# Performance work log

Measured on AMD Instinct MI355X. Metric: run time of the kernel, lower is better.

## Reference

```python
import jax, jax.numpy as jnp
import numpy as np

NUM_HIST = 4
INTERVAL = 5
PROG_THRESH = 2.0

B = 32          # scenarios
AGENTS_PER = 10 # agents per scenario
A = B * AGENTS_PER
T = 32          # future intervals
P = 20000       # polylines
NG = 2000       # polygons
L = 180         # raw trajectory length (L//INTERVAL = 36 >= T+1)


def setup_inputs() -> dict:
    key = jax.random.key(0)
    ks = jax.random.split(key, 8)
    polyline_batch = jnp.sort(jax.random.randint(ks[0], (P,), 0, B, dtype=jnp.int32))
    polyline_position = jax.random.normal(ks[1], (P, 2), dtype=jnp.float32) * 50.0
    polyline_heading = jax.random.uniform(ks[2], (P,), dtype=jnp.float32) * 2.0 * np.pi
    edge_row1 = jax.random.randint(ks[3], (P,), 0, NG, dtype=jnp.int32)
    polyline_to_polygon_edge_index = jnp.stack([jnp.arange(P, dtype=jnp.int32), edge_row1])
    polygon_on_route_mask = jax.random.randint(ks[4], (NG,), 0, 2) > 0
    agent_ptr = (jnp.arange(B + 1, dtype=jnp.int32) * AGENTS_PER)
    agent_infer_position = jax.random.normal(ks[5], (A, NUM_HIST + T, 2), dtype=jnp.float32) * 50.0
    agent_batch = jnp.repeat(jnp.arange(B, dtype=jnp.int32), AGENTS_PER)
    agent_position = jax.random.normal(ks[6], (A, L, 2), dtype=jnp.float32) * 50.0
    return {
        "polyline_batch": polyline_batch,
        "polyline_position": polyline_position,
        "polyline_heading": polyline_heading,
        "polyline_to_polygon_edge_index": polyline_to_polygon_edge_index,
        "polygon_on_route_mask": polygon_on_route_mask,
        "agent_ptr": agent_ptr,
        "agent_infer_position": agent_infer_position,
        "agent_batch": agent_batch,
        "agent_position": agent_position,
    }


def _local_x(points, centers, cos_h, sin_h):
    # points [E,2]; centers [P,2]; returns x_local, y_local each [E,P]
    dx = points[:, None, 0] - centers[None, :, 0]
    dy = points[:, None, 1] - centers[None, :, 1]
    x = cos_h[None, :] * dx + sin_h[None, :] * dy
    y = -sin_h[None, :] * dx + cos_h[None, :] * dy
    return x, y


def _progress(pos, pos_pre, pos_batch, poly_pos, cos_h, sin_h, on_route, poly_batch, t):
    # dense equivalent of mask-build -> dense_to_sparse -> gather -> scatter_min
    x, y = _local_x(pos, poly_pos, cos_h, sin_h)          # [E,P]
    x_pre, _ = _local_x(pos_pre, poly_pos, cos_h, sin_h)  # [E,P]
    dist = jnp.abs(y) * 10.0 + jnp.abs(x) + jnp.where(x > 0, 1000.0, 0.0)
    valid = on_route[None, :] & (pos_batch[:, None] == poly_batch[None, :])
    dist = jnp.where(valid, dist, jnp.inf)
    j = jnp.argmin(dist, axis=1)                          # first-min, matches scatter_min
    has = jnp.any(valid, axis=1)
    x_sel = jnp.take_along_axis(x, j[:, None], axis=1)[:, 0]
    x_pre_sel = jnp.take_along_axis(x_pre, j[:, None], axis=1)[:, 0]
    prog = jnp.where(has, x_sel - x_pre_sel, 0.0)
    return prog.reshape(-1, t).sum(axis=-1)


def reference(polyline_batch, polyline_position, polyline_heading,
              polyline_to_polygon_edge_index, polygon_on_route_mask,
              agent_ptr, agent_infer_position, agent_batch, agent_position):
    poly_on_route = polygon_on_route_mask[polyline_to_polygon_edge_index[1]]
    cos_h = jnp.cos(polyline_heading)
    sin_h = jnp.sin(polyline_heading)

    ego_index = agent_ptr[:-1]
    ip = agent_infer_position[ego_index]                  # [B, NUM_HIST+T, 2]
    t = ip.shape[1] - NUM_HIST
    ego_pos = ip[:, NUM_HIST:].reshape(-1, 2)
    ego_pos_pre = ip[:, NUM_HIST - 1:-1].reshape(-1, 2)
    ego_b = jnp.repeat(agent_batch[ego_index], t)

    progress = _progress(ego_pos, ego_pos_pre, ego_b, polyline_position,
                         cos_h, sin_h, poly_on_route, polyline_batch, t)

    expert = agent_position[ego_index, ::INTERVAL]        # [B, L//INTERVAL, 2]
    expert_pre = expert[:, -t - 1:-1].reshape(-1, 2)
    expert_cur = expert[:, -t:].reshape(-1, 2)
    expert_progress = _progress(expert_cur, expert_pre, ego_b, polyline_position,
                                cos_h, sin_h, poly_on_route, polyline_batch, t)

    reward = jnp.minimum(
        jnp.maximum(progress, PROG_THRESH) / jnp.maximum(expert_progress, PROG_THRESH),
        1.0)
    return reward
```

## Files before the change

### kernel.cpp

```cpp
#include <hip/hip_runtime.h>

#define NUM_HIST 4
#define T_STEPS 32
#define B_BATCH 32
#define AGENTS_PER 10
#define L_LEN 180
#define INTERVAL 5

__global__ void setup_kernel(const int* __restrict__ poly_batch,
                             const float* __restrict__ heading,
                             const int* __restrict__ edge,
                             const unsigned int* __restrict__ maskbuf,
                             float* __restrict__ cosv,
                             float* __restrict__ sinv,
                             int* __restrict__ onr,
                             int* __restrict__ starts,
                             float* __restrict__ acc,
                             int P)
{
    int t = blockIdx.x * blockDim.x + threadIdx.x;

    if (t < P) {
        bool bytemode = false;
        #pragma unroll 8
        for (int w = 0; w < 64; ++w) {
            if (maskbuf[w] & 0xFFFFFF00u) bytemode = true;
        }
        float h = heading[t];
        cosv[t] = cosf(h);
        sinv[t] = sinf(h);
        int g = edge[P + t];
        int on;
        if (bytemode) on = (((const unsigned char*)maskbuf)[g] != 0);
        else          on = (maskbuf[g] != 0);
        onr[t] = on;
    }

    if (t <= B_BATCH) {
        int lo = 0, hi = P;
        while (lo < hi) {
            int mid = (lo + hi) >> 1;
            if (poly_batch[mid] < t) lo = mid + 1; else hi = mid;
        }
        starts[t] = lo;
    }

    if (t < 2 * B_BATCH) acc[t] = 0.0f;
}

__global__ __launch_bounds__(64) void progress_kernel(
    const float* __restrict__ poly_pos,
    const float* __restrict__ cosv,
    const float* __restrict__ sinv,
    const int* __restrict__ onr,
    const int* __restrict__ starts,
    const int* __restrict__ agent_ptr,
    const int* __restrict__ agent_batch,
    const float* __restrict__ ipos,
    const float* __restrict__ apos,
    float* __restrict__ acc)
{
    const int q   = blockIdx.x;
    const int s   = q >> 10;
    const int row = q & 1023;
    const int b   = row >> 5;
    const int ts  = row & 31;
    const int lane = threadIdx.x;

    const int a  = agent_ptr[b];
    const int bq = agent_batch[a];

    float curx, cury, prex, prey;
    if (s == 0) {
        const float* base = ipos + (size_t)a * ((NUM_HIST + T_STEPS) * 2);
        curx = base[(NUM_HIST + ts) * 2 + 0];
        cury = base[(NUM_HIST + ts) * 2 + 1];
        prex = base[(NUM_HIST - 1 + ts) * 2 + 0];
        prey = base[(NUM_HIST - 1 + ts) * 2 + 1];
    } else {
        const float* base = apos + (size_t)a * (L_LEN * 2);
        curx = base[(4 + ts) * INTERVAL * 2 + 0];
        cury = base[(4 + ts) * INTERVAL * 2 + 1];
        prex = base[(3 + ts) * INTERVAL * 2 + 0];
        prey = base[(3 + ts) * INTERVAL * 2 + 1];
    }

    const int jb = starts[bq];
    const int je = starts[bq + 1];

    float bd = 3.402823466e38f;
    int   bj = 0x7FFFFFFF;

    for (int j = jb + lane; j < je; j += 64) {
        if (!onr[j]) continue;
        float px = poly_pos[2 * j + 0];
        float py = poly_pos[2 * j + 1];
        float c  = cosv[j];
        float sn = sinv[j];
        float dx = curx - px;
        float dy = cury - py;
        float x  = c * dx + sn * dy;
        float y  = -sn * dx + c * dy;
        float d  = fabsf(y) * 10.0f + fabsf(x) + (x > 0.0f ? 1000.0f : 0.0f);
        if (d < bd) { bd = d; bj = j; }
    }

    #pragma unroll
    for (int off = 32; off; off >>= 1) {
        float d2 = __shfl_xor(bd, off, 64);
        int   j2 = __shfl_xor(bj, off, 64);
        if (d2 < bd || (d2 == bd && j2 < bj)) { bd = d2; bj = j2; }
    }

    if (lane == 0) {
        float prog = 0.0f;
        if (bj != 0x7FFFFFFF) {
            float px = poly_pos[2 * bj + 0];
            float py = poly_pos[2 * bj + 1];
            float c  = cosv[bj];
            float sn = sinv[bj];
            float x_sel = c * (curx - px) + sn * (cury - py);
            float x_pre = c * (prex - px) + sn * (prey - py);
            prog = x_sel - x_pre;
        }
        atomicAdd(&acc[(s << 5) + b], prog);
    }
}

__global__ void finalize_kernel(const float* __restrict__ acc, float* __restrict__ out)
{
    int b = threadIdx.x;
    if (b < B_BATCH) {
        float p = acc[b];
        float e = acc[B_BATCH + b];
        out[b] = fminf(fmaxf(p, 2.0f) / fmaxf(e, 2.0f), 1.0f);
    }
}

extern "C" void kernel_launch(void* const* d_in, const int* in_sizes, int n_in,
                              void* d_out, int out_size, void* d_ws, size_t ws_size,
                              hipStream_t stream) {
    const int*   poly_batch  = (const int*)d_in[0];
    const float* poly_pos    = (const float*)d_in[1];
    const float* heading     = (const float*)d_in[2];
    const int*   edge        = (const int*)d_in[3];
    const unsigned int* mask = (const unsigned int*)d_in[4];
    const int*   agent_ptr   = (const int*)d_in[5];
    const float* ipos        = (const float*)d_in[6];
    const int*   agent_batch = (const int*)d_in[7];
    const float* apos        = (const float*)d_in[8];
    float* out = (float*)d_out;

    const int P = in_sizes[0];

    char* w = (char*)d_ws;
    float* cosv  = (float*)w;            w += (size_t)P * sizeof(float);
    float* sinv  = (float*)w;            w += (size_t)P * sizeof(float);
    int*   onr   = (int*)w;              w += (size_t)P * sizeof(int);
    int*   starts = (int*)w;             w += 64 * sizeof(int);
    float* acc   = (float*)w;

    int blocks = (P + 255) / 256;
    setup_kernel<<<blocks, 256, 0, stream>>>(poly_batch, heading, edge, mask,
                                             cosv, sinv, onr, starts, acc, P);

    progress_kernel<<<2 * B_BATCH * T_STEPS, 64, 0, stream>>>(
        poly_pos, cosv, sinv, onr, starts, agent_ptr, agent_batch, ipos, apos, acc);

    finalize_kernel<<<1, 64, 0, stream>>>(acc, out);
}
```

Measured before the change: 90.28 us.

## Fuse setup, progress and finalize into one per-scenario kernel with shared staging

```diff
diff --git a/kernel.cpp b/kernel.cpp
--- a/kernel.cpp
+++ b/kernel.cpp
@@ -3,136 +3,133 @@
 #define NUM_HIST 4
 #define T_STEPS 32
 #define B_BATCH 32
-#define AGENTS_PER 10
 #define L_LEN 180
 #define INTERVAL 5
+#define CHUNK 2048
+#define BT 1024
 
-__global__ void setup_kernel(const int* __restrict__ poly_batch,
-                             const float* __restrict__ heading,
-                             const int* __restrict__ edge,
-                             const unsigned int* __restrict__ maskbuf,
-                             float* __restrict__ cosv,
-                             float* __restrict__ sinv,
-                             int* __restrict__ onr,
-                             int* __restrict__ starts,
-                             float* __restrict__ acc,
-                             int P)
+__global__ __launch_bounds__(BT) void fused_progress_reward(
+    const int* __restrict__ pb,
+    const float* __restrict__ pp,
+    const float* __restrict__ hd,
+    const int* __restrict__ edge,
+    const unsigned int* __restrict__ mask,
+    const int* __restrict__ aptr,
+    const float* __restrict__ ipos,
+    const int* __restrict__ abatch,
+    const float* __restrict__ apos,
+    float* __restrict__ out,
+    int P)
 {
-    int t = blockIdx.x * blockDim.x + threadIdx.x;
+    __shared__ float4 stage[CHUNK];
+    __shared__ float progv[64];
+    __shared__ int sh_jb, sh_je;
 
-    if (t < P) {
-        bool bytemode = false;
-        #pragma unroll 8
-        for (int w = 0; w < 64; ++w) {
-            if (maskbuf[w] & 0xFFFFFF00u) bytemode = true;
+    const int tid = threadIdx.x;
+    const int b   = blockIdx.x;
+
+    bool bytemode = false;
+    for (int w = 0; w < 64; ++w) bytemode |= (mask[w] & 0xFFFFFF00u) != 0u;
+
+    const int a  = aptr[b];
+    const int bq = abatch[a];
+
+    if (tid == 0) { sh_jb = P; sh_je = P; }
+    __syncthreads();
+
+    {
+        int base = tid * 20;
+        if (base < P) {
+            int prev = (base == 0) ? -1 : pb[base - 1];
+            int lim  = min(base + 20, P);
+            for (int k = base; k < lim; ++k) {
+                int v = pb[k];
+                if (prev < bq     && v >= bq)     sh_jb = k;
+                if (prev < bq + 1 && v >= bq + 1) sh_je = k;
+                prev = v;
+            }
         }
-        float h = heading[t];
-        cosv[t] = cosf(h);
-        sinv[t] = sinf(h);
-        int g = edge[P + t];
-        int on;
-        if (bytemode) on = (((const unsigned char*)maskbuf)[g] != 0);
-        else          on = (maskbuf[g] != 0);
-        onr[t] = on;
     }
 
-    if (t <= B_BATCH) {
-        int lo = 0, hi = P;
-        while (lo < hi) {
-            int mid = (lo + hi) >> 1;
-            if (poly_batch[mid] < t) lo = mid + 1; else hi = mid;
-        }
-        starts[t] = lo;
+    const int qid = tid >> 4;
+    const int sub = tid & 15;
+    const int s   = qid >> 5;
+    const int ts  = qid & 31;
+
+    float cx, cy, px_, py_;
+    if (s == 0) {
+        const float* base = ipos + (size_t)a * ((NUM_HIST + T_STEPS) * 2);
+        cx  = base[(NUM_HIST + ts) * 2 + 0];
+        cy  = base[(NUM_HIST + ts) * 2 + 1];
+        px_ = base[(NUM_HIST - 1 + ts) * 2 + 0];
+        py_ = base[(NUM_HIST - 1 + ts) * 2 + 1];
+    } else {
+        const float* base = apos + (size_t)a * (L_LEN * 2);
+        cx  = base[(4 + ts) * INTERVAL * 2 + 0];
+        cy  = base[(4 + ts) * INTERVAL * 2 + 1];
+        px_ = base[(3 + ts) * INTERVAL * 2 + 0];
+        py_ = base[(3 + ts) * INTERVAL * 2 + 1];
     }
 
-    if (t < 2 * B_BATCH) acc[t] = 0.0f;
-}
+    __syncthreads();
+    const int jb = sh_jb;
+    const int je = sh_je;
 
-__global__ __launch_bounds__(64) void progress_kernel(
-    const float* __restrict__ poly_pos,
-    const float* __restrict__ cosv,
-    const float* __restrict__ sinv,
-    const int* __restrict__ onr,
-    const int* __restrict__ starts,
-    const int* __restrict__ agent_ptr,
-    const int* __restrict__ agent_batch,
-    const float* __restrict__ ipos,
-    const float* __restrict__ apos,
-    float* __restrict__ acc)
-{
-    const int q   = blockIdx.x;
-    const int s   = q >> 10;
-    const int row = q & 1023;
-    const int b   = row >> 5;
-    const int ts  = row & 31;
-    const int lane = threadIdx.x;
+    float bd = __builtin_inff();
+    int   bj = 0x7FFFFFFF;
+    float bc = 0.0f, bs = 0.0f;
 
-    const int a  = agent_ptr[b];
-    const int bq = agent_batch[a];
+    for (int c0 = jb; c0 < je; c0 += CHUNK) {
+        const int n = min(CHUNK, je - c0);
 
-    float curx, cury, prex, prey;
-    if (s == 0) {
-        const float* base = ipos + (size_t)a * ((NUM_HIST + T_STEPS) * 2);
-        curx = base[(NUM_HIST + ts) * 2 + 0];
-        cury = base[(NUM_HIST + ts) * 2 + 1];
-        prex = base[(NUM_HIST - 1 + ts) * 2 + 0];
-        prey = base[(NUM_HIST - 1 + ts) * 2 + 1];
-    } else {
-        const float* base = apos + (size_t)a * (L_LEN * 2);
-        curx = base[(4 + ts) * INTERVAL * 2 + 0];
-        cury = base[(4 + ts) * INTERVAL * 2 + 1];
-        prex = base[(3 + ts) * INTERVAL * 2 + 0];
-        prey = base[(3 + ts) * INTERVAL * 2 + 1];
-    }
+        for (int i = tid; i < n; i += BT) {
+            int j = c0 + i;
+            float h  = hd[j];
+            float cc = cosf(h);
+            float sn = sinf(h);
+            int g = edge[P + j];
+            bool on = bytemode ? (((const unsigned char*)mask)[g] != 0)
+                               : (mask[g] != 0u);
+            float px = pp[2 * j + 0];
+            float py = pp[2 * j + 1];
+            float tx = on ? (cc * px + sn * py) : __builtin_inff();
+            float ty = -sn * px + cc * py;
+            stage[i] = make_float4(cc, sn, tx, ty);
+        }
+        __syncthreads();
 
-    const int jb = starts[bq];
-    const int je = starts[bq + 1];
-
-    float bd = 3.402823466e38f;
-    int   bj = 0x7FFFFFFF;
-
-    for (int j = jb + lane; j < je; j += 64) {
-        if (!onr[j]) continue;
-        float px = poly_pos[2 * j + 0];
-        float py = poly_pos[2 * j + 1];
-        float c  = cosv[j];
-        float sn = sinv[j];
-        float dx = curx - px;
-        float dy = cury - py;
-        float x  = c * dx + sn * dy;
-        float y  = -sn * dx + c * dy;
-        float d  = fabsf(y) * 10.0f + fabsf(x) + (x > 0.0f ? 1000.0f : 0.0f);
-        if (d < bd) { bd = d; bj = j; }
+        for (int i = sub; i < n; i += 16) {
+            float4 e = stage[i];
+            float x = e.x * cx + e.y * cy - e.z;
+            float y = -e.y * cx + e.x * cy - e.w;
+            float d = fabsf(y) * 10.0f + fabsf(x) + (x > 0.0f ? 1000.0f : 0.0f);
+            int j = c0 + i;
+            if (d < bd) { bd = d; bj = j; bc = e.x; bs = e.y; }
+        }
+        __syncthreads();
     }
 
     #pragma unroll
-    for (int off = 32; off; off >>= 1) {
+    for (int off = 1; off < 16; off <<= 1) {
         float d2 = __shfl_xor(bd, off, 64);
         int   j2 = __shfl_xor(bj, off, 64);
-        if (d2 < bd || (d2 == bd && j2 < bj)) { bd = d2; bj = j2; }
+        float c2 = __shfl_xor(bc, off, 64);
+        float s2 = __shfl_xor(bs, off, 64);
+        if (d2 < bd || (d2 == bd && j2 < bj)) { bd = d2; bj = j2; bc = c2; bs = s2; }
     }
 
-    if (lane == 0) {
+    if (sub == 0) {
         float prog = 0.0f;
-        if (bj != 0x7FFFFFFF) {
-            float px = poly_pos[2 * bj + 0];
-            float py = poly_pos[2 * bj + 1];
-            float c  = cosv[bj];
-            float sn = sinv[bj];
-            float x_sel = c * (curx - px) + sn * (cury - py);
-            float x_pre = c * (prex - px) + sn * (prey - py);
-            prog = x_sel - x_pre;
-        }
-        atomicAdd(&acc[(s << 5) + b], prog);
+        if (bj != 0x7FFFFFFF)
+            prog = bc * (cx - px_) + bs * (cy - py_);
+        progv[qid] = prog;
     }
-}
+    __syncthreads();
 
-__global__ void finalize_kernel(const float* __restrict__ acc, float* __restrict__ out)
-{
-    int b = threadIdx.x;
-    if (b < B_BATCH) {
-        float p = acc[b];
-        float e = acc[B_BATCH + b];
+    if (tid == 0) {
+        float p = 0.0f, e = 0.0f;
+        #pragma unroll
+        for (int t = 0; t < T_STEPS; ++t) { p += progv[t]; e += progv[T_STEPS + t]; }
         out[b] = fminf(fmaxf(p, 2.0f) / fmaxf(e, 2.0f), 1.0f);
     }
 }
@@ -153,19 +150,7 @@
 
     const int P = in_sizes[0];
 
-    char* w = (char*)d_ws;
-    float* cosv  = (float*)w;            w += (size_t)P * sizeof(float);
-    float* sinv  = (float*)w;            w += (size_t)P * sizeof(float);
-    int*   onr   = (int*)w;              w += (size_t)P * sizeof(int);
-    int*   starts = (int*)w;             w += 64 * sizeof(int);
-    float* acc   = (float*)w;
-
-    int blocks = (P + 255) / 256;
-    setup_kernel<<<blocks, 256, 0, stream>>>(poly_batch, heading, edge, mask,
-                                             cosv, sinv, onr, starts, acc, P);
-
-    progress_kernel<<<2 * B_BATCH * T_STEPS, 64, 0, stream>>>(
-        poly_pos, cosv, sinv, onr, starts, agent_ptr, agent_batch, ipos, apos, acc);
-
-    finalize_kernel<<<1, 64, 0, stream>>>(acc, out);
+    fused_progress_reward<<<B_BATCH, BT, 0, stream>>>(
+        poly_batch, poly_pos, heading, edge, mask,
+        agent_ptr, ipos, agent_batch, apos, out, P);
 }
```

Measured after the change: 84.03 us. 1.07x faster.
